# Kernel tuning notes

Measured on AMD Instinct MI355X. Metric: run time of the kernel, lower is better.

Reference implementation:

```python
import jax, jax.numpy as jnp
import numpy as np

B, N, D = 4096, 200, 64
N_USERS, N_ITEMS, N_RATES = 100000, 100000, 6
EPS = 1e-10


def _linear_params(key, out_dim, in_dim):
    kw, kb = jax.random.split(key)
    bound = 1.0 / np.sqrt(in_dim)
    w = jax.random.uniform(kw, (out_dim, in_dim), jnp.float32, -bound, bound)
    b = jax.random.uniform(kb, (out_dim,), jnp.float32, -bound, bound)
    return w, b


def setup_inputs() -> dict:
    key = jax.random.key(0)
    ks = jax.random.split(key, 12)
    iids = jax.random.randint(ks[0], (B,), 0, N_ITEMS)
    uid_col = jax.random.randint(ks[1], (B, N), 0, N_USERS)  # 0 => padding
    rate_col = jax.random.randint(ks[2], (B, N), 0, N_RATES)
    i_user_pad = jnp.stack([uid_col, rate_col], axis=-1)  # [B, N, 2]
    user_emb = jax.random.normal(ks[3], (N_USERS, D), jnp.float32)
    item_emb = jax.random.normal(ks[4], (N_ITEMS, D), jnp.float32)
    rate_emb = jax.random.normal(ks[5], (N_RATES, D), jnp.float32)
    gu_w1, gu_b1 = _linear_params(ks[6], D, 2 * D)       # g_u layer1: 2D -> D (input_dim//2)
    gu_w2, gu_b2 = _linear_params(ks[7], D, D)           # g_u layer2: D -> D
    att_w1, att_b1 = _linear_params(ks[8], D, 2 * D)     # att layer1: 2D -> D
    att_w2, att_b2 = _linear_params(ks[9], 1, D)         # att layer2: D -> 1
    agg_w, agg_b = _linear_params(ks[10], D, D)          # aggre: D -> D
    return {"iids": iids, "i_user_pad": i_user_pad,
            "user_emb": user_emb, "item_emb": item_emb, "rate_emb": rate_emb,
            "gu_w1": gu_w1, "gu_b1": gu_b1, "gu_w2": gu_w2, "gu_b2": gu_b2,
            "att_w1": att_w1, "att_b1": att_b1, "att_w2": att_w2, "att_b2": att_b2,
            "agg_w": agg_w, "agg_b": agg_b}


def reference(iids, i_user_pad, user_emb, item_emb, rate_emb,
              gu_w1, gu_b1, gu_w2, gu_b2,
              att_w1, att_b1, att_w2, att_b2,
              agg_w, agg_b):
    uid = i_user_pad[:, :, 0]                       # [B, N]
    rid = i_user_pad[:, :, 1]                       # [B, N]
    p_t = user_emb[uid]                             # [B, N, D] neighbor-user gather
    i_user_er = rate_emb[rid]                       # [B, N, D] rating gather
    mask_i = (uid > 0).astype(p_t.dtype)            # [B, N]

    # g_u MLP: Linear(2D->D) + ReLU + Linear(D->D)
    x = jnp.concatenate([p_t, i_user_er], axis=2)   # [B, N, 2D]
    h = jax.nn.relu(jnp.einsum('bnd,kd->bnk', x, gu_w1) + gu_b1)
    f_jt = jnp.einsum('bnd,kd->bnk', h, gu_w2) + gu_b2  # [B, N, D]

    # masked broadcast of target item embedding
    q_j = mask_i[:, :, None] * item_emb[iids][:, None, :]  # [B, N, D]

    # attention MLP: Linear(2D->D) + ReLU + Linear(D->1)
    a = jnp.concatenate([f_jt, q_j], axis=2)        # [B, N, 2D]
    ah = jax.nn.relu(jnp.einsum('bnd,kd->bnk', a, att_w1) + att_b1)
    miu = (jnp.einsum('bnd,kd->bnk', ah, att_w2) + att_b2)[:, :, 0]  # [B, N]

    # exp-softmax over neighbors with masking (faithful to original, no max-subtract)
    miu = jnp.exp(miu) * mask_i
    miu = miu / (jnp.sum(miu, axis=1, keepdims=True) + EPS)

    # weighted sum aggregation + output Linear+ReLU
    agg = jnp.sum(miu[:, :, None] * f_jt, axis=1)   # [B, D]
    z_j = jax.nn.relu(agg @ agg_w.T + agg_b)        # [B, D]
    return z_j
```

## Files before the change

kernel.cpp:

```cpp
#include <hip/hip_runtime.h>
#include <hip/hip_bf16.h>

#define B_SZ 4096
#define N_SZ 200
#define NU_SZ 100000

#define OFF_BFRAG 0
#define OFF_AW1BT 12288
#define OFF_ERC   16384
#define OFF_QC    16768
#define OFF_AGG   278912
#define OFF_SC    541056
#define OFF_W32F  545152
#define OFF_AB1C  549248
#define OFF_H1U   549312
#define WS_NEED_BYTES ((size_t)(OFF_H1U + NU_SZ * 64) * 4)

typedef __attribute__((ext_vector_type(8))) __bf16 bf16x8;
typedef __attribute__((ext_vector_type(4))) __bf16 bf16x4;
typedef __attribute__((ext_vector_type(4))) float f32x4;
typedef __attribute__((ext_vector_type(4))) unsigned u32x4;

__device__ __forceinline__ void split2(float x, unsigned &hi, unsigned &lo) {
    unsigned u = __float_as_uint(x);
    hi = (u + 0x7FFFu + ((u >> 16) & 1u)) >> 16;
    float r = x - __uint_as_float(hi << 16);
    unsigned ul = __float_as_uint(r);
    lo = (ul + 0x7FFFu + ((ul >> 16) & 1u)) >> 16;
}

__device__ __forceinline__ unsigned packbf(float e0, float e1) {
    __bf16 h0 = (__bf16)e0, h1 = (__bf16)e1;
    return ((unsigned)__builtin_bit_cast(unsigned short, h1) << 16) |
           (unsigned)__builtin_bit_cast(unsigned short, h0);
}

__global__ void prep1(const float* __restrict__ gu_w1, const float* __restrict__ gu_b1,
                      const float* __restrict__ gu_w2, const float* __restrict__ att_w1,
                      const float* __restrict__ rate_emb, float* __restrict__ ws) {
    const int t0 = blockIdx.x * blockDim.x + threadIdx.x;
    const int stride = blockDim.x * gridDim.x;
    unsigned* wsu = (unsigned*)ws;
    for (int i = t0; i < 12288; i += stride) {
        int frag = i >> 8, within = i & 255, lane = within >> 2, r = within & 3;
        int hl = frag & 1, ct = (frag >> 1) & 3, kt = (frag >> 3) & 1, layer = frag >> 4;
        int col = ct * 16 + (lane & 15);
        int d0 = kt * 32 + 8 * (lane >> 4) + 2 * r;
        float w0, w1v;
        if (layer == 0)      { w0 = gu_w1[col * 128 + d0];  w1v = gu_w1[col * 128 + d0 + 1]; }
        else if (layer == 1) { w0 = gu_w2[col * 64 + d0];   w1v = gu_w2[col * 64 + d0 + 1]; }
        else                 { w0 = att_w1[col * 128 + d0]; w1v = att_w1[col * 128 + d0 + 1]; }
        unsigned h0, l0, h1, l1;
        split2(w0, h0, l0); split2(w1v, h1, l1);
        unsigned lo16 = hl ? l0 : h0;
        unsigned hi16 = hl ? l1 : h1;
        wsu[OFF_BFRAG + i] = lo16 | (hi16 << 16);
    }
    for (int i = t0; i < 4096; i += stride) {
        int d = i >> 6, k = i & 63;
        ws[OFF_AW1BT + i] = att_w1[k * 128 + 64 + d];
    }
    for (int i = t0; i < 384; i += stride) {
        int rr = i >> 6, k = i & 63;
        float a = gu_b1[k];
        for (int d = 0; d < 64; ++d)
            a += gu_w1[k * 128 + 64 + d] * rate_emb[rr * 64 + d];
        ws[OFF_ERC + i] = a;
    }
}

__global__ __launch_bounds__(256) void prep_w32(const float* __restrict__ att_w1,
                                                const float* __restrict__ gu_w2,
                                                const float* __restrict__ att_b1,
                                                const float* __restrict__ gu_b2,
                                                float* __restrict__ ws) {
    unsigned* w32f = (unsigned*)ws + OFF_W32F;
    int i = blockIdx.x * 256 + threadIdx.x;
    {
        int frag = i >> 8, within = i & 255, lane = within >> 2, r = within & 3;
        int hl = frag & 1, ct = (frag >> 1) & 3, kt = frag >> 3;
        int col = ct * 16 + (lane & 15);
        int d0 = kt * 32 + 8 * (lane >> 4) + 2 * r;
        if (hl == 0) {
            float w0 = 0.f, w1v = 0.f;
            for (int k2 = 0; k2 < 64; ++k2) {
                float a = att_w1[col * 128 + k2];
                w0  = fmaf(a, gu_w2[k2 * 64 + d0],     w0);
                w1v = fmaf(a, gu_w2[k2 * 64 + d0 + 1], w1v);
            }
            w32f[i] = packbf(w0, w1v);
        } else {
            w32f[i] = 0u;
        }
    }
    if (blockIdx.x == 0 && threadIdx.x < 64) {
        int k3 = threadIdx.x;
        float a = att_b1[k3];
        for (int k2 = 0; k2 < 64; ++k2)
            a = fmaf(att_w1[k3 * 128 + k2], gu_b2[k2], a);
        ws[OFF_AB1C + k3] = a;
    }
}

__global__ void prep2_qc(const int* __restrict__ iids, const float* __restrict__ item_emb,
                         const float* __restrict__ ws, float* __restrict__ qc) {
    int b = blockIdx.x, k = threadIdx.x;
    int iid = iids[b];
    const float* awbT = ws + OFF_AW1BT;
    const float* irow = item_emb + (size_t)iid * 64;
    float acc = 0.f;
    for (int d = 0; d < 64; ++d)
        acc = fmaf(awbT[d * 64 + k], irow[d], acc);
    qc[b * 64 + k] = acc;
}

#define LAYER_MFMA(LAYER_ID, ACC, AHARR, BFRAG, LANE)                            \
    _Pragma("unroll")                                                            \
    for (int ct = 0; ct < 4; ++ct) {                                             \
        const unsigned* fb = &BFRAG[((((LAYER_ID) * 2 + 0) * 4 + ct) * 2) * 256 + LANE * 4]; \
        u32x4 bh0 = *(const u32x4*)(fb + 0 * 256);                               \
        u32x4 bh1 = *(const u32x4*)(fb + 8 * 256);                               \
        ACC[ct] = __builtin_amdgcn_mfma_f32_16x16x32_bf16(AHARR[0], __builtin_bit_cast(bf16x8, bh0), ACC[ct], 0, 0, 0); \
        ACC[ct] = __builtin_amdgcn_mfma_f32_16x16x32_bf16(AHARR[1], __builtin_bit_cast(bf16x8, bh1), ACC[ct], 0, 0, 0); \
    }

__global__ __launch_bounds__(64) void prep_h1u(const float* __restrict__ user_emb,
                                               const float* __restrict__ ws,
                                               float* __restrict__ h1u) {
    __shared__ __align__(16) __bf16 XH[16 * 64];
    const int blk = blockIdx.x;
    const int lane = threadIdx.x;
    const int lrow = lane & 15;
    const int lgrp = lane >> 4;
    const int lcol = lane & 15;
    const unsigned* __restrict__ bfrag = (const unsigned*)ws + OFF_BFRAG;
    {
        const int dq = lane & 15;
        const int rowt = lane >> 4;
#pragma unroll
        for (int p = 0; p < 4; ++p) {
            int lr = p * 4 + rowt;
            int u  = blk * 16 + lr;
            float4 v = *(const float4*)(user_emb + (size_t)u * 64 + dq * 4);
            bf16x4 hv = { (__bf16)v.x, (__bf16)v.y, (__bf16)v.z, (__bf16)v.w };
            int g = dq >> 1;
            int idx = lr * 64 + ((g ^ (lr & 7)) << 3) + (dq & 1) * 4;
            *(bf16x4*)&XH[idx] = hv;
        }
    }
    bf16x8 AH[2];
    {
        int s = lrow & 7;
#pragma unroll
        for (int kt = 0; kt < 2; ++kt)
            AH[kt] = *(const bf16x8*)&XH[lrow * 64 + (((kt * 4 + lgrp) ^ s) << 3)];
    }
    f32x4 acc[4];
#pragma unroll
    for (int ct = 0; ct < 4; ++ct)
#pragma unroll
        for (int r = 0; r < 4; ++r) acc[ct][r] = 0.f;
    LAYER_MFMA(0, acc, AH, bfrag, lane)
#pragma unroll
    for (int ct = 0; ct < 4; ++ct)
#pragma unroll
        for (int r = 0; r < 4; ++r)
            h1u[(size_t)(blk * 16 + lgrp * 4 + r) * 64 + ct * 16 + lcol] = acc[ct][r];
}

__global__ __launch_bounds__(64) void fused_main3(
    const int* __restrict__ pad, const float* __restrict__ h1u,
    const float* __restrict__ gu_b2, const float* __restrict__ att_w2,
    const float* __restrict__ att_b2,
    const float* __restrict__ ws, float* __restrict__ aggbuf, float* __restrict__ scbuf) {

    __shared__ float erc_s[6 * 64];
    __shared__ float mask_s[16];
    __shared__ float b2_s[64], aw2_s[64], a1c_s[64], qc_s[64];

    const unsigned id = blockIdx.x;
    const int b = id / 13;
    const int t = id - b * 13;
    const int lane = threadIdx.x;
    const int lrow = lane & 15;
    const int lgrp = lane >> 4;
    const int lcol = lane & 15;
    const unsigned* __restrict__ bfrag = (const unsigned*)ws + OFF_BFRAG;
    const unsigned* __restrict__ w32f  = (const unsigned*)ws + OFF_W32F;
    const float ab2 = att_b2[0];

    b2_s[lane]  = gu_b2[lane];
    aw2_s[lane] = att_w2[lane];
    a1c_s[lane] = ws[OFF_AB1C + lane];
    qc_s[lane]  = ws[OFF_QC + b * 64 + lane];
#pragma unroll
    for (int i = 0; i < 6; ++i)
        erc_s[i * 64 + lane] = ws[OFF_ERC + i * 64 + lane];

    const int n = t * 16 + lrow;
    const bool valid = (n < N_SZ);
    int uid = 0, rid = 0;
    if (valid) {
        int2 pr = ((const int2*)pad)[b * N_SZ + n];
        uid = pr.x; rid = pr.y;
    }
    if (lane < 16)
        mask_s[lane] = (valid && uid > 0) ? 1.f : 0.f;

    bf16x8 AH[2];
#pragma unroll
    for (int kt = 0; kt < 2; ++kt) {
        const int ko = kt * 32 + lgrp * 8;
        float4 a = make_float4(0.f, 0.f, 0.f, 0.f), c = a;
        if (valid) {
            const float* hp = h1u + (size_t)uid * 64 + ko;
            a = *(const float4*)hp;
            c = *(const float4*)(hp + 4);
        }
        float4 ea = *(const float4*)&erc_s[rid * 64 + ko];
        float4 ec = *(const float4*)&erc_s[rid * 64 + ko + 4];
        float h0 = fmaxf(a.x + ea.x, 0.f), h1 = fmaxf(a.y + ea.y, 0.f);
        float h2 = fmaxf(a.z + ea.z, 0.f), h3 = fmaxf(a.w + ea.w, 0.f);
        float h4 = fmaxf(c.x + ec.x, 0.f), h5 = fmaxf(c.y + ec.y, 0.f);
        float h6 = fmaxf(c.z + ec.z, 0.f), h7 = fmaxf(c.w + ec.w, 0.f);
        u32x4 hq = { packbf(h0, h1), packbf(h2, h3), packbf(h4, h5), packbf(h6, h7) };
        AH[kt] = __builtin_bit_cast(bf16x8, hq);
    }

    f32x4 f_reg[4];
#pragma unroll
    for (int ct = 0; ct < 4; ++ct) {
        float bb = b2_s[ct * 16 + lcol];
#pragma unroll
        for (int r = 0; r < 4; ++r) f_reg[ct][r] = bb;
    }
    LAYER_MFMA(1, f_reg, AH, bfrag, lane)

    float maskr[4];
#pragma unroll
    for (int r = 0; r < 4; ++r) maskr[r] = mask_s[lgrp * 4 + r];
    f32x4 acc3[4];
#pragma unroll
    for (int ct = 0; ct < 4; ++ct) {
        int k = ct * 16 + lcol;
        float bb = a1c_s[k], qq = qc_s[k];
#pragma unroll
        for (int r = 0; r < 4; ++r) acc3[ct][r] = fmaf(maskr[r], qq, bb);
    }
    LAYER_MFMA(0, acc3, AH, w32f, lane)

    float pm[4] = { 0.f, 0.f, 0.f, 0.f };
#pragma unroll
    for (int ct = 0; ct < 4; ++ct) {
        float w2v = aw2_s[ct * 16 + lcol];
#pragma unroll
        for (int r = 0; r < 4; ++r)
            pm[r] = fmaf(fmaxf(acc3[ct][r], 0.f), w2v, pm[r]);
    }
#pragma unroll
    for (int off = 1; off <= 8; off <<= 1) {
#pragma unroll
        for (int r = 0; r < 4; ++r) pm[r] += __shfl_xor(pm[r], off);
    }
    float aggr[4];
    float swave = 0.f;
    {
        float miur[4];
#pragma unroll
        for (int r = 0; r < 4; ++r) {
            miur[r] = __expf(pm[r] + ab2) * maskr[r];
            swave += miur[r];
        }
#pragma unroll
        for (int ct = 0; ct < 4; ++ct) {
            float a = 0.f;
#pragma unroll
            for (int r = 0; r < 4; ++r)
                a = fmaf(miur[r], f_reg[ct][r], a);
            aggr[ct] = a;
        }
    }

#pragma unroll
    for (int ct = 0; ct < 4; ++ct) {
        float v = aggr[ct];
        v += __shfl_xor(v, 16);
        v += __shfl_xor(v, 32);
        aggr[ct] = v;
    }
    swave += __shfl_xor(swave, 16);
    swave += __shfl_xor(swave, 32);
    if (lane < 16) {
#pragma unroll
        for (int ct = 0; ct < 4; ++ct)
            atomicAdd(&aggbuf[b * 64 + ct * 16 + lane], aggr[ct]);
    }
    if (lane == 0)
        atomicAdd(&scbuf[b], swave);
}

__global__ __launch_bounds__(64) void fused_main1(
    const int* __restrict__ pad, const float* __restrict__ user_emb,
    const float* __restrict__ gu_b2, const float* __restrict__ att_b1,
    const float* __restrict__ att_w2, const float* __restrict__ att_b2,
    const float* __restrict__ ws, float* __restrict__ aggbuf, float* __restrict__ scbuf) {

    __shared__ __align__(16) __bf16 XH[16 * 64];
    __shared__ float erc_s[6 * 65];
    __shared__ int   rid_s[16];
    __shared__ float mask_s[16];
    __shared__ float b2_s[64], aw2_s[64], ab1_s[64], qc_s[64];

    const unsigned id = blockIdx.x;
    const int b = id / 13;
    const int t = id - b * 13;
    const int lane = threadIdx.x;
    const int lrow = lane & 15;
    const int lgrp = lane >> 4;
    const int lcol = lane & 15;
    const unsigned* __restrict__ bfrag = (const unsigned*)ws + OFF_BFRAG;
    const float ab2 = att_b2[0];

    b2_s[lane]  = gu_b2[lane];
    aw2_s[lane] = att_w2[lane];
    ab1_s[lane] = att_b1[lane];
    qc_s[lane]  = ws[OFF_QC + b * 64 + lane];
#pragma unroll
    for (int i = 0; i < 6; ++i) {
        int j = i * 64 + lane;
        erc_s[(j >> 6) * 65 + (j & 63)] = ws[OFF_ERC + j];
    }
    {
        const int dq = lane & 15;
        const int rowt = lane >> 4;
#pragma unroll
        for (int p = 0; p < 4; ++p) {
            int lr = p * 4 + rowt;
            int n  = t * 16 + lr;
            int uid = 0, rid = 0;
            float4 v = make_float4(0.f, 0.f, 0.f, 0.f);
            if (n < N_SZ) {
                int2 pr = ((const int2*)pad)[b * N_SZ + n];
                uid = pr.x; rid = pr.y;
                v = *(const float4*)(user_emb + (size_t)uid * 64 + dq * 4);
            }
            bf16x4 hv = { (__bf16)v.x, (__bf16)v.y, (__bf16)v.z, (__bf16)v.w };
            int g = dq >> 1;
            int idx = lr * 64 + ((g ^ (lr & 7)) << 3) + (dq & 1) * 4;
            *(bf16x4*)&XH[idx] = hv;
            if (dq == 0) {
                rid_s[lr]  = (n < N_SZ) ? rid : 0;
                mask_s[lr] = (n < N_SZ && uid > 0) ? 1.f : 0.f;
            }
        }
    }
    auto loadA = [&](bf16x8 A[2]) {
        int s = lrow & 7;
#pragma unroll
        for (int kt = 0; kt < 2; ++kt)
            A[kt] = *(const bf16x8*)&XH[lrow * 64 + (((kt * 4 + lgrp) ^ s) << 3)];
    };
    {
        bf16x8 AH[2];
        loadA(AH);
        int ridr[4];
#pragma unroll
        for (int r = 0; r < 4; ++r) ridr[r] = rid_s[lgrp * 4 + r];
        f32x4 acc[4];
#pragma unroll
        for (int ct = 0; ct < 4; ++ct) {
            int k = ct * 16 + lcol;
#pragma unroll
            for (int r = 0; r < 4; ++r) acc[ct][r] = erc_s[ridr[r] * 65 + k];
        }
        LAYER_MFMA(0, acc, AH, bfrag, lane)
#pragma unroll
        for (int ct = 0; ct < 4; ++ct) {
            int col = ct * 16 + lcol;
#pragma unroll
            for (int r = 0; r < 4; ++r) {
                float hv = fmaxf(acc[ct][r], 0.f);
                int ln = lgrp * 4 + r;
                int idx = ln * 64 + (((col >> 3) ^ (ln & 7)) << 3) + (col & 7);
                XH[idx] = (__bf16)hv;
            }
        }
    }
    f32x4 f_reg[4];
    {
        bf16x8 AH[2];
        loadA(AH);
#pragma unroll
        for (int ct = 0; ct < 4; ++ct) {
            float bb = b2_s[ct * 16 + lcol];
#pragma unroll
            for (int r = 0; r < 4; ++r) f_reg[ct][r] = bb;
        }
        LAYER_MFMA(1, f_reg, AH, bfrag, lane)
#pragma unroll
        for (int ct = 0; ct < 4; ++ct) {
            int col = ct * 16 + lcol;
#pragma unroll
            for (int r = 0; r < 4; ++r) {
                int ln = lgrp * 4 + r;
                int idx = ln * 64 + (((col >> 3) ^ (ln & 7)) << 3) + (col & 7);
                XH[idx] = (__bf16)f_reg[ct][r];
            }
        }
    }
    float aggr[4];
    float swave = 0.f;
    {
        bf16x8 AH[2];
        loadA(AH);
        float maskr[4];
#pragma unroll
        for (int r = 0; r < 4; ++r) maskr[r] = mask_s[lgrp * 4 + r];
        f32x4 acc[4];
#pragma unroll
        for (int ct = 0; ct < 4; ++ct) {
            int k = ct * 16 + lcol;
            float bb = ab1_s[k], qq = qc_s[k];
#pragma unroll
            for (int r = 0; r < 4; ++r) acc[ct][r] = fmaf(maskr[r], qq, bb);
        }
        LAYER_MFMA(2, acc, AH, bfrag, lane)
        float pm[4] = { 0.f, 0.f, 0.f, 0.f };
#pragma unroll
        for (int ct = 0; ct < 4; ++ct) {
            float w2v = aw2_s[ct * 16 + lcol];
#pragma unroll
            for (int r = 0; r < 4; ++r)
                pm[r] = fmaf(fmaxf(acc[ct][r], 0.f), w2v, pm[r]);
        }
#pragma unroll
        for (int off = 1; off <= 8; off <<= 1) {
#pragma unroll
            for (int r = 0; r < 4; ++r) pm[r] += __shfl_xor(pm[r], off);
        }
        float miur[4];
#pragma unroll
        for (int r = 0; r < 4; ++r) {
            miur[r] = __expf(pm[r] + ab2) * maskr[r];
            swave += miur[r];
        }
#pragma unroll
        for (int ct = 0; ct < 4; ++ct) {
            float a = 0.f;
#pragma unroll
            for (int r = 0; r < 4; ++r)
                a = fmaf(miur[r], f_reg[ct][r], a);
            aggr[ct] = a;
        }
    }
#pragma unroll
    for (int ct = 0; ct < 4; ++ct) {
        float v = aggr[ct];
        v += __shfl_xor(v, 16);
        v += __shfl_xor(v, 32);
        aggr[ct] = v;
    }
    swave += __shfl_xor(swave, 16);
    swave += __shfl_xor(swave, 32);
    if (lane < 16) {
#pragma unroll
        for (int ct = 0; ct < 4; ++ct)
            atomicAdd(&aggbuf[b * 64 + ct * 16 + lane], aggr[ct]);
    }
    if (lane == 0)
        atomicAdd(&scbuf[b], swave);
}

__global__ __launch_bounds__(256) void final_z(const float* __restrict__ aggbuf,
                                               const float* __restrict__ scbuf,
                                               const float* __restrict__ agg_w,
                                               const float* __restrict__ agg_b,
                                               float* __restrict__ out) {
    __shared__ float aws[64 * 65];
    int t = threadIdx.x;
    for (int idx = t; idx < 4096; idx += 256)
        aws[(idx >> 6) * 65 + (idx & 63)] = agg_w[idx];
    __syncthreads();
    int g = t >> 6, k = t & 63;
    for (int bi = 0; bi < 2; ++bi) {
        int b = blockIdx.x * 8 + g * 2 + bi;
        const float* arow = aggbuf + b * 64;
        float inv = 1.f / (scbuf[b] + 1e-10f);
        float dot = 0.f;
        for (int d = 0; d < 64; ++d)
            dot = fmaf(aws[k * 65 + d], arow[d], dot);
        out[b * 64 + k] = fmaxf(fmaf(inv, dot, agg_b[k]), 0.f);
    }
}

extern "C" void kernel_launch(void* const* d_in, const int* in_sizes, int n_in,
                              void* d_out, int out_size, void* d_ws, size_t ws_size,
                              hipStream_t stream) {
    const int*   iids     = (const int*)d_in[0];
    const int*   pad      = (const int*)d_in[1];
    const float* user_emb = (const float*)d_in[2];
    const float* item_emb = (const float*)d_in[3];
    const float* rate_emb = (const float*)d_in[4];
    const float* gu_w1    = (const float*)d_in[5];
    const float* gu_b1    = (const float*)d_in[6];
    const float* gu_w2    = (const float*)d_in[7];
    const float* gu_b2    = (const float*)d_in[8];
    const float* att_w1   = (const float*)d_in[9];
    const float* att_b1   = (const float*)d_in[10];
    const float* att_w2   = (const float*)d_in[11];
    const float* att_b2   = (const float*)d_in[12];
    const float* agg_w    = (const float*)d_in[13];
    const float* agg_b    = (const float*)d_in[14];
    float* ws  = (float*)d_ws;
    float* out = (float*)d_out;

    hipLaunchKernelGGL(prep1, dim3(32), dim3(256), 0, stream,
                       gu_w1, gu_b1, gu_w2, att_w1, rate_emb, ws);
    hipLaunchKernelGGL(prep2_qc, dim3(B_SZ), dim3(64), 0, stream,
                       iids, item_emb, ws, ws + OFF_QC);
    hipMemsetAsync(ws + OFF_AGG, 0, (size_t)(B_SZ * 64 + B_SZ) * sizeof(float), stream);

    if (ws_size >= WS_NEED_BYTES) {
        hipLaunchKernelGGL(prep_w32, dim3(16), dim3(256), 0, stream,
                           att_w1, gu_w2, att_b1, gu_b2, ws);
        hipLaunchKernelGGL(prep_h1u, dim3(NU_SZ / 16), dim3(64), 0, stream,
                           user_emb, ws, ws + OFF_H1U);
        hipLaunchKernelGGL(fused_main3, dim3(B_SZ * 13), dim3(64), 0, stream,
                           pad, ws + OFF_H1U, gu_b2, att_w2, att_b2,
                           ws, ws + OFF_AGG, ws + OFF_SC);
    } else {
        hipLaunchKernelGGL(fused_main1, dim3(B_SZ * 13), dim3(64), 0, stream,
                           pad, user_emb, gu_b2, att_b1, att_w2, att_b2,
                           ws, ws + OFF_AGG, ws + OFF_SC);
    }
    hipLaunchKernelGGL(final_z, dim3(B_SZ / 8), dim3(256), 0, stream,
                       ws + OFF_AGG, ws + OFF_SC, agg_w, agg_b, out);
}
```

Measured before the change: 105.1 us.

## Process two neighbor tiles per block and drop shared-memory staging

The main fused kernel now handles two 16-neighbor tiles per 64-thread block (7 blocks per batch row instead of 13). Per-block setup and the atomic reductions into the aggregate buffers are shared across both tiles. The shared-memory staging of biases, rating-embedding contributions and masks is replaced with direct register and global loads, so the block needs no LDS. This reduces block count, atomics and setup overhead, at the cost of less parallelism per block and extra global loads for the mask values.

```diff
diff --git a/kernel.cpp b/kernel.cpp
--- a/kernel.cpp
+++ b/kernel.cpp
@@ -168,118 +168,116 @@
             h1u[(size_t)(blk * 16 + lgrp * 4 + r) * 64 + ct * 16 + lcol] = acc[ct][r];
 }
 
-__global__ __launch_bounds__(64) void fused_main3(
+__global__ __launch_bounds__(64) void fused_main4(
     const int* __restrict__ pad, const float* __restrict__ h1u,
     const float* __restrict__ gu_b2, const float* __restrict__ att_w2,
     const float* __restrict__ att_b2,
     const float* __restrict__ ws, float* __restrict__ aggbuf, float* __restrict__ scbuf) {
 
-    __shared__ float erc_s[6 * 64];
-    __shared__ float mask_s[16];
-    __shared__ float b2_s[64], aw2_s[64], a1c_s[64], qc_s[64];
-
     const unsigned id = blockIdx.x;
-    const int b = id / 13;
-    const int t = id - b * 13;
+    const int b = id / 7;
+    const int c = id - b * 7;
     const int lane = threadIdx.x;
     const int lrow = lane & 15;
     const int lgrp = lane >> 4;
     const int lcol = lane & 15;
     const unsigned* __restrict__ bfrag = (const unsigned*)ws + OFF_BFRAG;
     const unsigned* __restrict__ w32f  = (const unsigned*)ws + OFF_W32F;
+    const float* __restrict__ ercp = ws + OFF_ERC;
     const float ab2 = att_b2[0];
 
-    b2_s[lane]  = gu_b2[lane];
-    aw2_s[lane] = att_w2[lane];
-    a1c_s[lane] = ws[OFF_AB1C + lane];
-    qc_s[lane]  = ws[OFF_QC + b * 64 + lane];
-#pragma unroll
-    for (int i = 0; i < 6; ++i)
-        erc_s[i * 64 + lane] = ws[OFF_ERC + i * 64 + lane];
-
-    const int n = t * 16 + lrow;
-    const bool valid = (n < N_SZ);
-    int uid = 0, rid = 0;
-    if (valid) {
-        int2 pr = ((const int2*)pad)[b * N_SZ + n];
-        uid = pr.x; rid = pr.y;
-    }
-    if (lane < 16)
-        mask_s[lane] = (valid && uid > 0) ? 1.f : 0.f;
-
-    bf16x8 AH[2];
-#pragma unroll
-    for (int kt = 0; kt < 2; ++kt) {
-        const int ko = kt * 32 + lgrp * 8;
-        float4 a = make_float4(0.f, 0.f, 0.f, 0.f), c = a;
-        if (valid) {
-            const float* hp = h1u + (size_t)uid * 64 + ko;
-            a = *(const float4*)hp;
-            c = *(const float4*)(hp + 4);
-        }
-        float4 ea = *(const float4*)&erc_s[rid * 64 + ko];
-        float4 ec = *(const float4*)&erc_s[rid * 64 + ko + 4];
-        float h0 = fmaxf(a.x + ea.x, 0.f), h1 = fmaxf(a.y + ea.y, 0.f);
-        float h2 = fmaxf(a.z + ea.z, 0.f), h3 = fmaxf(a.w + ea.w, 0.f);
-        float h4 = fmaxf(c.x + ec.x, 0.f), h5 = fmaxf(c.y + ec.y, 0.f);
-        float h6 = fmaxf(c.z + ec.z, 0.f), h7 = fmaxf(c.w + ec.w, 0.f);
-        u32x4 hq = { packbf(h0, h1), packbf(h2, h3), packbf(h4, h5), packbf(h6, h7) };
-        AH[kt] = __builtin_bit_cast(bf16x8, hq);
-    }
-
-    f32x4 f_reg[4];
-#pragma unroll
-    for (int ct = 0; ct < 4; ++ct) {
-        float bb = b2_s[ct * 16 + lcol];
-#pragma unroll
-        for (int r = 0; r < 4; ++r) f_reg[ct][r] = bb;
-    }
-    LAYER_MFMA(1, f_reg, AH, bfrag, lane)
-
-    float maskr[4];
-#pragma unroll
-    for (int r = 0; r < 4; ++r) maskr[r] = mask_s[lgrp * 4 + r];
-    f32x4 acc3[4];
+    float b2v[4], aw2v[4], a1cv[4], qcv[4];
 #pragma unroll
     for (int ct = 0; ct < 4; ++ct) {
         int k = ct * 16 + lcol;
-        float bb = a1c_s[k], qq = qc_s[k];
-#pragma unroll
-        for (int r = 0; r < 4; ++r) acc3[ct][r] = fmaf(maskr[r], qq, bb);
-    }
-    LAYER_MFMA(0, acc3, AH, w32f, lane)
-
-    float pm[4] = { 0.f, 0.f, 0.f, 0.f };
-#pragma unroll
-    for (int ct = 0; ct < 4; ++ct) {
-        float w2v = aw2_s[ct * 16 + lcol];
-#pragma unroll
-        for (int r = 0; r < 4; ++r)
-            pm[r] = fmaf(fmaxf(acc3[ct][r], 0.f), w2v, pm[r]);
-    }
-#pragma unroll
-    for (int off = 1; off <= 8; off <<= 1) {
-#pragma unroll
-        for (int r = 0; r < 4; ++r) pm[r] += __shfl_xor(pm[r], off);
-    }
-    float aggr[4];
+        b2v[ct]  = gu_b2[k];
+        aw2v[ct] = att_w2[k];
+        a1cv[ct] = ws[OFF_AB1C + k];
+        qcv[ct]  = ws[OFF_QC + b * 64 + k];
+    }
+
+    float aggr[4] = { 0.f, 0.f, 0.f, 0.f };
     float swave = 0.f;
-    {
-        float miur[4];
-#pragma unroll
-        for (int r = 0; r < 4; ++r) {
-            miur[r] = __expf(pm[r] + ab2) * maskr[r];
-            swave += miur[r];
-        }
-#pragma unroll
-        for (int ct = 0; ct < 4; ++ct) {
-            float a = 0.f;
-#pragma unroll
-            for (int r = 0; r < 4; ++r)
-                a = fmaf(miur[r], f_reg[ct][r], a);
-            aggr[ct] = a;
-        }
-    }
+
+#define TILE_BODY(TT)                                                            \
+    {                                                                            \
+        const int n = (TT) * 16 + lrow;                                          \
+        const bool valid = (n < N_SZ);                                           \
+        int uid = 0, rid = 0;                                                    \
+        if (valid) {                                                             \
+            int2 pr = ((const int2*)pad)[b * N_SZ + n];                          \
+            uid = pr.x; rid = pr.y;                                              \
+        }                                                                        \
+        float maskr[4];                                                          \
+        _Pragma("unroll")                                                        \
+        for (int r = 0; r < 4; ++r) {                                            \
+            int nr = (TT) * 16 + lgrp * 4 + r;                                   \
+            int uidr = (nr < N_SZ) ? pad[2 * (b * N_SZ + nr)] : 0;               \
+            maskr[r] = (nr < N_SZ && uidr > 0) ? 1.f : 0.f;                      \
+        }                                                                        \
+        bf16x8 AH[2];                                                            \
+        _Pragma("unroll")                                                        \
+        for (int kt = 0; kt < 2; ++kt) {                                         \
+            const int ko = kt * 32 + lgrp * 8;                                   \
+            float4 a = make_float4(0.f, 0.f, 0.f, 0.f), cc = a;                  \
+            if (valid) {                                                         \
+                const float* hp = h1u + (size_t)uid * 64 + ko;                   \
+                a  = *(const float4*)hp;                                         \
+                cc = *(const float4*)(hp + 4);                                   \
+            }                                                                    \
+            float4 ea = *(const float4*)&ercp[rid * 64 + ko];                    \
+            float4 ec = *(const float4*)&ercp[rid * 64 + ko + 4];                \
+            float h0 = fmaxf(a.x + ea.x, 0.f), h1 = fmaxf(a.y + ea.y, 0.f);      \
+            float h2 = fmaxf(a.z + ea.z, 0.f), h3 = fmaxf(a.w + ea.w, 0.f);      \
+            float h4 = fmaxf(cc.x + ec.x, 0.f), h5 = fmaxf(cc.y + ec.y, 0.f);    \
+            float h6 = fmaxf(cc.z + ec.z, 0.f), h7 = fmaxf(cc.w + ec.w, 0.f);    \
+            u32x4 hq = { packbf(h0, h1), packbf(h2, h3),                         \
+                         packbf(h4, h5), packbf(h6, h7) };                       \
+            AH[kt] = __builtin_bit_cast(bf16x8, hq);                             \
+        }                                                                        \
+        f32x4 f_reg[4];                                                          \
+        _Pragma("unroll")                                                        \
+        for (int ct = 0; ct < 4; ++ct) {                                         \
+            _Pragma("unroll")                                                    \
+            for (int r = 0; r < 4; ++r) f_reg[ct][r] = b2v[ct];                  \
+        }                                                                        \
+        LAYER_MFMA(1, f_reg, AH, bfrag, lane)                                    \
+        f32x4 acc3[4];                                                           \
+        _Pragma("unroll")                                                        \
+        for (int ct = 0; ct < 4; ++ct) {                                         \
+            _Pragma("unroll")                                                    \
+            for (int r = 0; r < 4; ++r)                                          \
+                acc3[ct][r] = fmaf(maskr[r], qcv[ct], a1cv[ct]);                 \
+        }                                                                        \
+        LAYER_MFMA(0, acc3, AH, w32f, lane)                                      \
+        float pm[4] = { 0.f, 0.f, 0.f, 0.f };                                    \
+        _Pragma("unroll")                                                        \
+        for (int ct = 0; ct < 4; ++ct) {                                         \
+            _Pragma("unroll")                                                    \
+            for (int r = 0; r < 4; ++r)                                          \
+                pm[r] = fmaf(fmaxf(acc3[ct][r], 0.f), aw2v[ct], pm[r]);          \
+        }                                                                        \
+        _Pragma("unroll")                                                        \
+        for (int off = 1; off <= 8; off <<= 1) {                                 \
+            _Pragma("unroll")                                                    \
+            for (int r = 0; r < 4; ++r) pm[r] += __shfl_xor(pm[r], off);         \
+        }                                                                        \
+        float miur[4];                                                           \
+        _Pragma("unroll")                                                        \
+        for (int r = 0; r < 4; ++r) {                                            \
+            miur[r] = __expf(pm[r] + ab2) * maskr[r];                            \
+            swave += miur[r];                                                    \
+        }                                                                        \
+        _Pragma("unroll")                                                        \
+        for (int ct = 0; ct < 4; ++ct) {                                         \
+            _Pragma("unroll")                                                    \
+            for (int r = 0; r < 4; ++r)                                          \
+                aggr[ct] = fmaf(miur[r], f_reg[ct][r], aggr[ct]);                \
+        }                                                                        \
+    }
+
+    TILE_BODY(2 * c)
+    if (c < 6) TILE_BODY(2 * c + 1)
 
 #pragma unroll
     for (int ct = 0; ct < 4; ++ct) {
@@ -525,7 +523,7 @@
                            att_w1, gu_w2, att_b1, gu_b2, ws);
         hipLaunchKernelGGL(prep_h1u, dim3(NU_SZ / 16), dim3(64), 0, stream,
                            user_emb, ws, ws + OFF_H1U);
-        hipLaunchKernelGGL(fused_main3, dim3(B_SZ * 13), dim3(64), 0, stream,
+        hipLaunchKernelGGL(fused_main4, dim3(B_SZ * 7), dim3(64), 0, stream,
                            pad, ws + OFF_H1U, gu_b2, att_w2, att_b2,
                            ws, ws + OFF_AGG, ws + OFF_SC);
     } else {
```

Result: slower. 136.4 us (+29.8%).

## Merge prep kernels, fold memset into prep, drop LDS staging in main kernel

Applied to the files above, without the earlier changes.

Combines prep1, prep_w32 and the accumulator memset into one prep_all kernel. The qc computation is folded into the h1u prep launch as extra blocks. In the main kernel, the small per-block constants and the mask are loaded straight into registers instead of being staged through shared memory, and the rating table is read from global memory. The aim is fewer launches and less LDS/barrier overhead, at the cost of redundant global loads per lane and a longer serial prep kernel.

```diff
diff --git a/kernel.cpp b/kernel.cpp
--- a/kernel.cpp
+++ b/kernel.cpp
@@ -35,9 +35,11 @@
            (unsigned)__builtin_bit_cast(unsigned short, h0);
 }
 
-__global__ void prep1(const float* __restrict__ gu_w1, const float* __restrict__ gu_b1,
-                      const float* __restrict__ gu_w2, const float* __restrict__ att_w1,
-                      const float* __restrict__ rate_emb, float* __restrict__ ws) {
+__global__ __launch_bounds__(256) void prep_all(
+    const float* __restrict__ gu_w1, const float* __restrict__ gu_b1,
+    const float* __restrict__ gu_w2, const float* __restrict__ att_w1,
+    const float* __restrict__ att_b1, const float* __restrict__ gu_b2,
+    const float* __restrict__ rate_emb, float* __restrict__ ws) {
     const int t0 = blockIdx.x * blockDim.x + threadIdx.x;
     const int stride = blockDim.x * gridDim.x;
     unsigned* wsu = (unsigned*)ws;
@@ -67,16 +69,7 @@
             a += gu_w1[k * 128 + 64 + d] * rate_emb[rr * 64 + d];
         ws[OFF_ERC + i] = a;
     }
-}
-
-__global__ __launch_bounds__(256) void prep_w32(const float* __restrict__ att_w1,
-                                                const float* __restrict__ gu_w2,
-                                                const float* __restrict__ att_b1,
-                                                const float* __restrict__ gu_b2,
-                                                float* __restrict__ ws) {
-    unsigned* w32f = (unsigned*)ws + OFF_W32F;
-    int i = blockIdx.x * 256 + threadIdx.x;
-    {
+    for (int i = t0; i < 4096; i += stride) {
         int frag = i >> 8, within = i & 255, lane = within >> 2, r = within & 3;
         int hl = frag & 1, ct = (frag >> 1) & 3, kt = frag >> 3;
         int col = ct * 16 + (lane & 15);
@@ -88,30 +81,19 @@
                 w0  = fmaf(a, gu_w2[k2 * 64 + d0],     w0);
                 w1v = fmaf(a, gu_w2[k2 * 64 + d0 + 1], w1v);
             }
-            w32f[i] = packbf(w0, w1v);
+            wsu[OFF_W32F + i] = packbf(w0, w1v);
         } else {
-            w32f[i] = 0u;
-        }
-    }
-    if (blockIdx.x == 0 && threadIdx.x < 64) {
-        int k3 = threadIdx.x;
-        float a = att_b1[k3];
+            wsu[OFF_W32F + i] = 0u;
+        }
+    }
+    for (int i = t0; i < 64; i += stride) {
+        float a = att_b1[i];
         for (int k2 = 0; k2 < 64; ++k2)
-            a = fmaf(att_w1[k3 * 128 + k2], gu_b2[k2], a);
-        ws[OFF_AB1C + k3] = a;
-    }
-}
-
-__global__ void prep2_qc(const int* __restrict__ iids, const float* __restrict__ item_emb,
-                         const float* __restrict__ ws, float* __restrict__ qc) {
-    int b = blockIdx.x, k = threadIdx.x;
-    int iid = iids[b];
-    const float* awbT = ws + OFF_AW1BT;
-    const float* irow = item_emb + (size_t)iid * 64;
-    float acc = 0.f;
-    for (int d = 0; d < 64; ++d)
-        acc = fmaf(awbT[d * 64 + k], irow[d], acc);
-    qc[b * 64 + k] = acc;
+            a = fmaf(att_w1[i * 128 + k2], gu_b2[k2], a);
+        ws[OFF_AB1C + i] = a;
+    }
+    for (int i = t0; i < B_SZ * 64; i += stride) ws[OFF_AGG + i] = 0.f;
+    for (int i = t0; i < B_SZ; i += stride)      ws[OFF_SC + i] = 0.f;
 }
 
 #define LAYER_MFMA(LAYER_ID, ACC, AHARR, BFRAG, LANE)                            \
@@ -124,12 +106,26 @@
         ACC[ct] = __builtin_amdgcn_mfma_f32_16x16x32_bf16(AHARR[1], __builtin_bit_cast(bf16x8, bh1), ACC[ct], 0, 0, 0); \
     }
 
-__global__ __launch_bounds__(64) void prep_h1u(const float* __restrict__ user_emb,
-                                               const float* __restrict__ ws,
-                                               float* __restrict__ h1u) {
-    __shared__ __align__(16) __bf16 XH[16 * 64];
+template <int DO_H1U>
+__global__ __launch_bounds__(64) void prep_h1u_qc(
+    const float* __restrict__ user_emb, const int* __restrict__ iids,
+    const float* __restrict__ item_emb, const float* __restrict__ ws,
+    float* __restrict__ h1u, float* __restrict__ qc) {
     const int blk = blockIdx.x;
     const int lane = threadIdx.x;
+    const int nh = DO_H1U ? (NU_SZ / 16) : 0;
+    if (blk >= nh) {
+        int b = blk - nh;
+        int iid = iids[b];
+        const float* awbT = ws + OFF_AW1BT;
+        const float* irow = item_emb + (size_t)iid * 64;
+        float acc = 0.f;
+        for (int d = 0; d < 64; ++d)
+            acc = fmaf(awbT[d * 64 + lane], irow[d], acc);
+        qc[b * 64 + lane] = acc;
+        return;
+    }
+    __shared__ __align__(16) __bf16 XH[16 * 64];
     const int lrow = lane & 15;
     const int lgrp = lane >> 4;
     const int lcol = lane & 15;
@@ -168,15 +164,11 @@
             h1u[(size_t)(blk * 16 + lgrp * 4 + r) * 64 + ct * 16 + lcol] = acc[ct][r];
 }
 
-__global__ __launch_bounds__(64) void fused_main3(
+__global__ __launch_bounds__(64) void fused_main5(
     const int* __restrict__ pad, const float* __restrict__ h1u,
     const float* __restrict__ gu_b2, const float* __restrict__ att_w2,
     const float* __restrict__ att_b2,
     const float* __restrict__ ws, float* __restrict__ aggbuf, float* __restrict__ scbuf) {
-
-    __shared__ float erc_s[6 * 64];
-    __shared__ float mask_s[16];
-    __shared__ float b2_s[64], aw2_s[64], a1c_s[64], qc_s[64];
 
     const unsigned id = blockIdx.x;
     const int b = id / 13;
@@ -187,15 +179,18 @@
     const int lcol = lane & 15;
     const unsigned* __restrict__ bfrag = (const unsigned*)ws + OFF_BFRAG;
     const unsigned* __restrict__ w32f  = (const unsigned*)ws + OFF_W32F;
+    const float* __restrict__ ercp = ws + OFF_ERC;
     const float ab2 = att_b2[0];
 
-    b2_s[lane]  = gu_b2[lane];
-    aw2_s[lane] = att_w2[lane];
-    a1c_s[lane] = ws[OFF_AB1C + lane];
-    qc_s[lane]  = ws[OFF_QC + b * 64 + lane];
-#pragma unroll
-    for (int i = 0; i < 6; ++i)
-        erc_s[i * 64 + lane] = ws[OFF_ERC + i * 64 + lane];
+    float b2v[4], aw2v[4], a1cv[4], qcv[4];
+#pragma unroll
+    for (int ct = 0; ct < 4; ++ct) {
+        int k = ct * 16 + lcol;
+        b2v[ct]  = gu_b2[k];
+        aw2v[ct] = att_w2[k];
+        a1cv[ct] = ws[OFF_AB1C + k];
+        qcv[ct]  = ws[OFF_QC + b * 64 + k];
+    }
 
     const int n = t * 16 + lrow;
     const bool valid = (n < N_SZ);
@@ -204,25 +199,30 @@
         int2 pr = ((const int2*)pad)[b * N_SZ + n];
         uid = pr.x; rid = pr.y;
     }
-    if (lane < 16)
-        mask_s[lane] = (valid && uid > 0) ? 1.f : 0.f;
+    float maskr[4];
+#pragma unroll
+    for (int r = 0; r < 4; ++r) {
+        int nr = t * 16 + lgrp * 4 + r;
+        int uidr = (nr < N_SZ) ? pad[2 * (b * N_SZ + nr)] : 0;
+        maskr[r] = (nr < N_SZ && uidr > 0) ? 1.f : 0.f;
+    }
 
     bf16x8 AH[2];
 #pragma unroll
     for (int kt = 0; kt < 2; ++kt) {
         const int ko = kt * 32 + lgrp * 8;
-        float4 a = make_float4(0.f, 0.f, 0.f, 0.f), c = a;
+        float4 a = make_float4(0.f, 0.f, 0.f, 0.f), cc = a;
         if (valid) {
             const float* hp = h1u + (size_t)uid * 64 + ko;
-            a = *(const float4*)hp;
-            c = *(const float4*)(hp + 4);
-        }
-        float4 ea = *(const float4*)&erc_s[rid * 64 + ko];
-        float4 ec = *(const float4*)&erc_s[rid * 64 + ko + 4];
+            a  = *(const float4*)hp;
+            cc = *(const float4*)(hp + 4);
+        }
+        float4 ea = *(const float4*)&ercp[rid * 64 + ko];
+        float4 ec = *(const float4*)&ercp[rid * 64 + ko + 4];
         float h0 = fmaxf(a.x + ea.x, 0.f), h1 = fmaxf(a.y + ea.y, 0.f);
         float h2 = fmaxf(a.z + ea.z, 0.f), h3 = fmaxf(a.w + ea.w, 0.f);
-        float h4 = fmaxf(c.x + ec.x, 0.f), h5 = fmaxf(c.y + ec.y, 0.f);
-        float h6 = fmaxf(c.z + ec.z, 0.f), h7 = fmaxf(c.w + ec.w, 0.f);
+        float h4 = fmaxf(cc.x + ec.x, 0.f), h5 = fmaxf(cc.y + ec.y, 0.f);
+        float h6 = fmaxf(cc.z + ec.z, 0.f), h7 = fmaxf(cc.w + ec.w, 0.f);
         u32x4 hq = { packbf(h0, h1), packbf(h2, h3), packbf(h4, h5), packbf(h6, h7) };
         AH[kt] = __builtin_bit_cast(bf16x8, hq);
     }
@@ -230,32 +230,26 @@
     f32x4 f_reg[4];
 #pragma unroll
     for (int ct = 0; ct < 4; ++ct) {
-        float bb = b2_s[ct * 16 + lcol];
-#pragma unroll
-        for (int r = 0; r < 4; ++r) f_reg[ct][r] = bb;
+#pragma unroll
+        for (int r = 0; r < 4; ++r) f_reg[ct][r] = b2v[ct];
     }
     LAYER_MFMA(1, f_reg, AH, bfrag, lane)
 
-    float maskr[4];
-#pragma unroll
-    for (int r = 0; r < 4; ++r) maskr[r] = mask_s[lgrp * 4 + r];
     f32x4 acc3[4];
 #pragma unroll
     for (int ct = 0; ct < 4; ++ct) {
-        int k = ct * 16 + lcol;
-        float bb = a1c_s[k], qq = qc_s[k];
-#pragma unroll
-        for (int r = 0; r < 4; ++r) acc3[ct][r] = fmaf(maskr[r], qq, bb);
+#pragma unroll
+        for (int r = 0; r < 4; ++r)
+            acc3[ct][r] = fmaf(maskr[r], qcv[ct], a1cv[ct]);
     }
     LAYER_MFMA(0, acc3, AH, w32f, lane)
 
     float pm[4] = { 0.f, 0.f, 0.f, 0.f };
 #pragma unroll
     for (int ct = 0; ct < 4; ++ct) {
-        float w2v = aw2_s[ct * 16 + lcol];
 #pragma unroll
         for (int r = 0; r < 4; ++r)
-            pm[r] = fmaf(fmaxf(acc3[ct][r], 0.f), w2v, pm[r]);
+            pm[r] = fmaf(fmaxf(acc3[ct][r], 0.f), aw2v[ct], pm[r]);
     }
 #pragma unroll
     for (int off = 1; off <= 8; off <<= 1) {
@@ -514,21 +508,18 @@
     float* ws  = (float*)d_ws;
     float* out = (float*)d_out;
 
-    hipLaunchKernelGGL(prep1, dim3(32), dim3(256), 0, stream,
-                       gu_w1, gu_b1, gu_w2, att_w1, rate_emb, ws);
-    hipLaunchKernelGGL(prep2_qc, dim3(B_SZ), dim3(64), 0, stream,
-                       iids, item_emb, ws, ws + OFF_QC);
-    hipMemsetAsync(ws + OFF_AGG, 0, (size_t)(B_SZ * 64 + B_SZ) * sizeof(float), stream);
+    hipLaunchKernelGGL(prep_all, dim3(64), dim3(256), 0, stream,
+                       gu_w1, gu_b1, gu_w2, att_w1, att_b1, gu_b2, rate_emb, ws);
 
     if (ws_size >= WS_NEED_BYTES) {
-        hipLaunchKernelGGL(prep_w32, dim3(16), dim3(256), 0, stream,
-                           att_w1, gu_w2, att_b1, gu_b2, ws);
-        hipLaunchKernelGGL(prep_h1u, dim3(NU_SZ / 16), dim3(64), 0, stream,
-                           user_emb, ws, ws + OFF_H1U);
-        hipLaunchKernelGGL(fused_main3, dim3(B_SZ * 13), dim3(64), 0, stream,
+        hipLaunchKernelGGL((prep_h1u_qc<1>), dim3(NU_SZ / 16 + B_SZ), dim3(64), 0, stream,
+                           user_emb, iids, item_emb, ws, ws + OFF_H1U, ws + OFF_QC);
+        hipLaunchKernelGGL(fused_main5, dim3(B_SZ * 13), dim3(64), 0, stream,
                            pad, ws + OFF_H1U, gu_b2, att_w2, att_b2,
                            ws, ws + OFF_AGG, ws + OFF_SC);
     } else {
+        hipLaunchKernelGGL((prep_h1u_qc<0>), dim3(B_SZ), dim3(64), 0, stream,
+                           user_emb, iids, item_emb, ws, ws + OFF_QC, ws + OFF_QC);
         hipLaunchKernelGGL(fused_main1, dim3(B_SZ * 13), dim3(64), 0, stream,
                            pad, user_emb, gu_b2, att_b1, att_w2, att_b2,
                            ws, ws + OFF_AGG, ws + OFF_SC);
```

New measurement: 118.6 us. 12.9% more time.
